# Performance work log

Measured on AMD Instinct MI355X. Metric: run time of the kernel, lower is better.

Reference implementation:

```python
import jax, jax.numpy as jnp
import numpy as np

TOKENS, HIDDEN = 2048, 1024
N_EXPERTS, INTER, TOPK = 8, 2816, 2
RENORMALIZE = True


def setup_inputs() -> dict:
    key = jax.random.key(0)
    k1, k2, k3, k4 = jax.random.split(key, 4)
    x = jax.random.normal(k1, (TOKENS, HIDDEN), dtype=jnp.float32)
    gating_output = jax.random.normal(k2, (TOKENS, N_EXPERTS), dtype=jnp.float32)
    # stacked gate_proj+up_proj per expert: [E, 2*I, H]
    w1 = jax.random.normal(k3, (N_EXPERTS, 2 * INTER, HIDDEN), dtype=jnp.float32) * 0.02
    # down_proj per expert: [E, H, I]
    w2 = jax.random.normal(k4, (N_EXPERTS, HIDDEN, INTER), dtype=jnp.float32) * 0.02
    return {"x": x, "gating_output": gating_output, "w1": w1, "w2": w2}


def _moe(x, gating_output, w1, w2):
    # fused_topk: softmax over router logits, then top-k, then renormalize
    probs = jax.nn.softmax(gating_output, axis=-1)              # [T, E]
    topk_w, topk_ids = jax.lax.top_k(probs, TOPK)                # [T, K]
    if RENORMALIZE:
        topk_w = topk_w / jnp.sum(topk_w, axis=-1, keepdims=True)
    # fused_experts: gate/up proj -> SiLU(gate)*up -> down proj, per expert
    h = jnp.einsum('th,eih->tei', x, w1)                         # [T, E, 2I]
    gate, up = h[..., :INTER], h[..., INTER:]
    act = jax.nn.silu(gate) * up                                 # [T, E, I]
    out_e = jnp.einsum('tei,ehi->teh', act, w2)                  # [T, E, H]
    # combine: gather selected experts and weight them
    sel = jnp.take_along_axis(out_e, topk_ids[:, :, None], axis=1)  # [T, K, H]
    return jnp.sum(sel * topk_w[:, :, None].astype(sel.dtype), axis=1)  # [T, H]


def reference(x, gating_output, w1, w2):
    return _moe(x, gating_output, w1, w2)
```

## Files before the change

kernel.cpp:

```cpp
#include <hip/hip_runtime.h>
#include <hip/hip_bf16.h>

#define TOKENS 2048
#define HIDDEN 1024
#define NEXP   8
#define INTER  2816
#define N1     5632
#define ROWCAP 5120
#define MT     40
#define NT1    44
#define NT2    8
#define SPLITK 2
#define CONVB  2048

typedef __attribute__((ext_vector_type(8))) short short8;
typedef __attribute__((ext_vector_type(4))) float f32x4;

typedef unsigned int __attribute__((address_space(1))) as1_uint;
typedef unsigned int __attribute__((address_space(3))) as3_uint;

__device__ __forceinline__ void gload16(const void* g, void* l) {
  __builtin_amdgcn_global_load_lds((const as1_uint*)g, (as3_uint*)l, 16, 0, 0);
}

__device__ __forceinline__ unsigned short f2bf(float f) {
  unsigned u = __float_as_uint(f);
  u += 0x7fff + ((u >> 16) & 1);
  return (unsigned short)(u >> 16);
}
__device__ __forceinline__ float bf2f(unsigned short h) {
  return __uint_as_float(((unsigned)h) << 16);
}
__device__ __forceinline__ unsigned short bfs(float x) {
  __hip_bfloat16 h = __float2bfloat16(x);
  return *reinterpret_cast<unsigned short*>(&h);
}
__device__ __forceinline__ short8 pack8(f32x4 lo, f32x4 hi) {
  short8 o;
  o[0] = (short)bfs(lo[0]); o[1] = (short)bfs(lo[1]); o[2] = (short)bfs(lo[2]); o[3] = (short)bfs(lo[3]);
  o[4] = (short)bfs(hi[0]); o[5] = (short)bfs(hi[1]); o[6] = (short)bfs(hi[2]); o[7] = (short)bfs(hi[3]);
  return o;
}

__global__ void k_routing(const float* __restrict__ gate, int* __restrict__ ctrl,
                          int* __restrict__ tkid, float* __restrict__ tkw) {
  int t = blockIdx.x * blockDim.x + threadIdx.x;
  if (t >= TOKENS) return;
  float l[8];
#pragma unroll
  for (int i = 0; i < 8; i++) l[i] = gate[t * 8 + i];
  int i0 = 0; float m0 = l[0];
#pragma unroll
  for (int i = 1; i < 8; i++) if (l[i] > m0) { m0 = l[i]; i0 = i; }
  int i1 = -1; float m1 = -3.4e38f;
#pragma unroll
  for (int i = 0; i < 8; i++) if (i != i0 && l[i] > m1) { m1 = l[i]; i1 = i; }
  float e  = __expf(m1 - m0);
  float w0 = 1.f / (1.f + e);
  float w1 = e / (1.f + e);
  tkid[2 * t] = i0; tkid[2 * t + 1] = i1;
  tkw[2 * t] = w0;  tkw[2 * t + 1] = w1;
  atomicAdd(&ctrl[i0], 1);
  atomicAdd(&ctrl[i1], 1);
}

__global__ void k_base(int* ctrl) {
  if (threadIdx.x == 0) {
    int a = 0;
    for (int e = 0; e < 8; e++) { ctrl[16 + e] = a; a += ((ctrl[e] + 127) >> 7) << 7; }
  }
}

__global__ void k_fill(int* __restrict__ ctrl, const int* __restrict__ tkid,
                       int* __restrict__ rtok, int* __restrict__ trow) {
  int t = blockIdx.x * blockDim.x + threadIdx.x;
  if (t >= TOKENS) return;
#pragma unroll
  for (int k = 0; k < 2; k++) {
    int e = tkid[2 * t + k];
    int pos = atomicAdd(&ctrl[8 + e], 1);
    int row = ctrl[16 + e] + pos;
    rtok[row] = t;
    trow[2 * t + k] = row;
  }
}

__global__ void k_prep(const float* __restrict__ x, const int* __restrict__ ctrl,
                       const int* __restrict__ rtok, unsigned short* __restrict__ Abf,
                       const float* __restrict__ w2, unsigned short* __restrict__ w2b) {
  int b = blockIdx.x;
  if (b < ROWCAP) {
    int row = b;
    int e = -1, local = 0;
    for (int i = 0; i < 8; i++) {
      int bb = ctrl[16 + i], p = ((ctrl[i] + 127) >> 7) << 7;
      if (row >= bb && row < bb + p) { e = i; local = row - bb; break; }
    }
    if (e < 0) return;
    int tid = threadIdx.x;
    unsigned short* dst = Abf + (size_t)row * HIDDEN;
    if (local < ctrl[e]) {
      int t = rtok[row];
      float4 v = ((const float4*)(x + (size_t)t * HIDDEN))[tid];
      ushort4 o; o.x = f2bf(v.x); o.y = f2bf(v.y); o.z = f2bf(v.z); o.w = f2bf(v.w);
      ((ushort4*)dst)[tid] = o;
    } else {
      ushort4 z; z.x = 0; z.y = 0; z.z = 0; z.w = 0;
      ((ushort4*)dst)[tid] = z;
    }
  } else {
    const int n8 = NEXP * HIDDEN * INTER / 8;
    int i = (b - ROWCAP) * blockDim.x + threadIdx.x;
    int stride = CONVB * blockDim.x;
    for (; i < n8; i += stride) {
      float4 a = ((const float4*)w2)[2 * i];
      float4 c = ((const float4*)w2)[2 * i + 1];
      union { ushort us[8]; uint4 v; } o;
      o.us[0] = f2bf(a.x); o.us[1] = f2bf(a.y); o.us[2] = f2bf(a.z); o.us[3] = f2bf(a.w);
      o.us[4] = f2bf(c.x); o.us[5] = f2bf(c.y); o.us[6] = f2bf(c.z); o.us[7] = f2bf(c.w);
      ((uint4*)w2b)[i] = o.v;
    }
  }
}

__device__ __forceinline__ int tile_lookup(const int* ctrl, int mt, int* ml) {
  int a0 = 0;
  for (int i = 0; i < 8; i++) {
    int pt = (ctrl[i] + 127) >> 7;
    if (mt < a0 + pt) { *ml = mt - a0; return i; }
    a0 += pt;
  }
  return -1;
}

__global__ __launch_bounds__(256, 3) void k_gemm1(const float* __restrict__ w1,
    const unsigned short* __restrict__ Abf, unsigned short* __restrict__ act,
    const int* __restrict__ ctrl) {
  union __align__(16) LdsU {
    struct { unsigned char A[16384]; unsigned char Bf[32768]; } st;
    unsigned short hb[128 * 132];
  };
  __shared__ LdsU lds;
  int bid = blockIdx.x;
  int wg = (bid & 7) * (NT1 * MT / 8) + (bid >> 3);
  int nt = wg / MT, mt = wg % MT;
  int ml; int e = tile_lookup(ctrl, mt, &ml);
  if (e < 0) return;
  int tid = threadIdx.x, lane = tid & 63, wid = tid >> 6, wr = wid >> 1, wc = wid & 1;
  int rbase = ctrl[16 + e] + ml * 128;
  const unsigned char* Ab = (const unsigned char*)(Abf + (size_t)rbase * HIDDEN);
  const unsigned char* Bw = (const unsigned char*)(w1 + (size_t)e * N1 * HIDDEN);
  int l3 = lane >> 3, l4 = lane >> 4, l15 = lane & 15;
  int swzA = ((lane & 7) ^ l3) << 4;

  unsigned aoff[4], boff[8];
#pragma unroll
  for (int i = 0; i < 4; i++) {
    int g = wid * 4 + i;
    aoff[i] = (unsigned)(g * 8 + l3) * (HIDDEN * 2) + swzA;
  }
#pragma unroll
  for (int i = 0; i < 8; i++) {
    int r = (wid * 8 + i) * 4 + l4;
    int grow = (r < 64) ? nt * 64 + r : INTER + nt * 64 + (r - 64);
    boff[i] = (unsigned)grow * (HIDDEN * 4) + ((l15 ^ (r & 15)) << 4);
  }

  f32x4 acc[4][4];
  f32x4 zero = {0.f, 0.f, 0.f, 0.f};
#pragma unroll
  for (int i = 0; i < 4; i++)
#pragma unroll
    for (int j = 0; j < 4; j++) acc[i][j] = zero;

  for (int kk = 0; kk < HIDDEN / 64; ++kk) {
#pragma unroll
    for (int i = 0; i < 4; i++)
      gload16(Ab + (size_t)aoff[i] + kk * 128, &lds.st.A[(wid * 4 + i) * 1024]);
#pragma unroll
    for (int i = 0; i < 8; i++)
      gload16(Bw + (size_t)boff[i] + kk * 256, &lds.st.Bf[(wid * 8 + i) * 1024]);
    __syncthreads();
#pragma unroll
    for (int ks = 0; ks < 2; ++ks) {
      short8 a[4], b[4];
#pragma unroll
      for (int mi = 0; mi < 4; mi++) {
        int row = wr * 64 + mi * 16 + l15;
        int koff = ks * 64 + (l4 << 4);
        a[mi] = *(const short8*)&lds.st.A[row * 128 + (koff ^ ((row & 7) << 4))];
      }
#pragma unroll
      for (int ni = 0; ni < 4; ni++) {
        int r = wc * 64 + ni * 16 + l15;
        int c = ks * 8 + l4 * 2;
        f32x4 lo = *(const f32x4*)&lds.st.Bf[r * 256 + ((c ^ (r & 15)) << 4)];
        f32x4 hi = *(const f32x4*)&lds.st.Bf[r * 256 + (((c + 1) ^ (r & 15)) << 4)];
        b[ni] = pack8(lo, hi);
      }
#pragma unroll
      for (int mi = 0; mi < 4; mi++)
#pragma unroll
        for (int ni = 0; ni < 4; ni++)
          acc[mi][ni] = __builtin_amdgcn_mfma_f32_16x16x32_bf16(a[mi], b[ni], acc[mi][ni], 0, 0, 0);
    }
    __syncthreads();
  }
#pragma unroll
  for (int mi = 0; mi < 4; mi++)
#pragma unroll
    for (int ni = 0; ni < 4; ni++)
#pragma unroll
      for (int r = 0; r < 4; r++) {
        int row = wr * 64 + mi * 16 + (l4 << 2) + r;
        int col = wc * 64 + ni * 16 + l15;
        lds.hb[row * 132 + col] = f2bf(acc[mi][ni][r]);
      }
  __syncthreads();
  {
    int r = tid >> 1, ch = (tid & 1) * 32;
    unsigned short* orow = act + (size_t)(rbase + r) * INTER + nt * 64 + ch;
    const unsigned short* hrow = &lds.hb[r * 132];
#pragma unroll
    for (int j = 0; j < 32; j += 4) {
      ushort4 o;
#pragma unroll
      for (int q = 0; q < 4; q++) {
        float g = bf2f(hrow[ch + j + q]);
        float u = bf2f(hrow[64 + ch + j + q]);
        float s = g / (1.f + __expf(-g));
        ((unsigned short*)&o)[q] = f2bf(s * u);
      }
      *(ushort4*)(orow + j) = o;
    }
  }
}

__global__ __launch_bounds__(256, 4) void k_gemm2b(const unsigned short* __restrict__ w2b,
    const unsigned short* __restrict__ act, float* __restrict__ Pb,
    const int* __restrict__ ctrl) {
  struct __align__(16) Lds2 { unsigned char A[16384]; unsigned char B[16384]; };
  __shared__ Lds2 lds;
  int bid = blockIdx.x;
  int wg = (bid & 7) * (NT2 * MT * SPLITK / 8) + (bid >> 3);
  int mt = wg % MT;
  int p = wg / MT;
  int z = p & 1, nt = p >> 1;
  int ml; int e = tile_lookup(ctrl, mt, &ml);
  if (e < 0) return;
  int tid = threadIdx.x, lane = tid & 63, wid = tid >> 6, wr = wid >> 1, wc = wid & 1;
  int rbase = ctrl[16 + e] + ml * 128;
  const int KST = (INTER / 64) / SPLITK;
  const unsigned char* Ab = (const unsigned char*)(act + (size_t)rbase * INTER) + (size_t)z * KST * 128;
  const unsigned char* Bb = (const unsigned char*)(w2b + (size_t)e * HIDDEN * INTER) + (size_t)z * KST * 128;
  int l3 = lane >> 3, l4 = lane >> 4, l15 = lane & 15;
  int swz = ((lane & 7) ^ l3) << 4;

  unsigned aoff[4], boff[4];
#pragma unroll
  for (int i = 0; i < 4; i++) {
    int g = wid * 4 + i;
    aoff[i] = (unsigned)(g * 8 + l3) * (INTER * 2) + swz;
    boff[i] = (unsigned)(nt * 128 + g * 8 + l3) * (INTER * 2) + swz;
  }

  f32x4 acc[4][4];
  f32x4 zero = {0.f, 0.f, 0.f, 0.f};
#pragma unroll
  for (int i = 0; i < 4; i++)
#pragma unroll
    for (int j = 0; j < 4; j++) acc[i][j] = zero;

  for (int kk = 0; kk < KST; ++kk) {
#pragma unroll
    for (int i = 0; i < 4; i++)
      gload16(Ab + (size_t)aoff[i] + kk * 128, &lds.A[(wid * 4 + i) * 1024]);
#pragma unroll
    for (int i = 0; i < 4; i++)
      gload16(Bb + (size_t)boff[i] + kk * 128, &lds.B[(wid * 4 + i) * 1024]);
    __syncthreads();
#pragma unroll
    for (int ks = 0; ks < 2; ++ks) {
      short8 a[4], b[4];
#pragma unroll
      for (int mi = 0; mi < 4; mi++) {
        int row = wr * 64 + mi * 16 + l15;
        int koff = ks * 64 + (l4 << 4);
        a[mi] = *(const short8*)&lds.A[row * 128 + (koff ^ ((row & 7) << 4))];
      }
#pragma unroll
      for (int ni = 0; ni < 4; ni++) {
        int row = wc * 64 + ni * 16 + l15;
        int koff = ks * 64 + (l4 << 4);
        b[ni] = *(const short8*)&lds.B[row * 128 + (koff ^ ((row & 7) << 4))];
      }
#pragma unroll
      for (int mi = 0; mi < 4; mi++)
#pragma unroll
        for (int ni = 0; ni < 4; ni++)
          acc[mi][ni] = __builtin_amdgcn_mfma_f32_16x16x32_bf16(a[mi], b[ni], acc[mi][ni], 0, 0, 0);
    }
    __syncthreads();
  }
  float* P = Pb + (size_t)z * ROWCAP * HIDDEN;
#pragma unroll
  for (int mi = 0; mi < 4; mi++)
#pragma unroll
    for (int ni = 0; ni < 4; ni++) {
      int col = nt * 128 + wc * 64 + ni * 16 + l15;
#pragma unroll
      for (int r = 0; r < 4; r++) {
        int row = rbase + wr * 64 + mi * 16 + (l4 << 2) + r;
        P[(size_t)row * HIDDEN + col] = acc[mi][ni][r];
      }
    }
}

__global__ void k_finish(const float* __restrict__ Pb,
                         const int* __restrict__ trow, const float* __restrict__ tkw,
                         float* __restrict__ out) {
  int t = blockIdx.x, c = threadIdx.x;
  const float* P0 = Pb;
  const float* P1 = Pb + (size_t)ROWCAP * HIDDEN;
  int r0 = trow[2 * t], r1 = trow[2 * t + 1];
  float w0 = tkw[2 * t], w1 = tkw[2 * t + 1];
  float4 a0 = ((const float4*)(P0 + (size_t)r0 * HIDDEN))[c];
  float4 b0 = ((const float4*)(P1 + (size_t)r0 * HIDDEN))[c];
  float4 a1 = ((const float4*)(P0 + (size_t)r1 * HIDDEN))[c];
  float4 b1 = ((const float4*)(P1 + (size_t)r1 * HIDDEN))[c];
  float4 o;
  o.x = w0 * (a0.x + b0.x) + w1 * (a1.x + b1.x);
  o.y = w0 * (a0.y + b0.y) + w1 * (a1.y + b1.y);
  o.z = w0 * (a0.z + b0.z) + w1 * (a1.z + b1.z);
  o.w = w0 * (a0.w + b0.w) + w1 * (a1.w + b1.w);
  ((float4*)(out + (size_t)t * HIDDEN))[c] = o;
}

extern "C" void kernel_launch(void* const* d_in, const int* in_sizes, int n_in,
                              void* d_out, int out_size, void* d_ws, size_t ws_size,
                              hipStream_t stream) {
  const float* x      = (const float*)d_in[0];
  const float* gating = (const float*)d_in[1];
  const float* w1     = (const float*)d_in[2];
  const float* w2     = (const float*)d_in[3];
  float* out = (float*)d_out;
  char* ws = (char*)d_ws;

  int*   ctrl = (int*)ws;
  int*   tkid = (int*)(ws + 4096);
  float* tkw  = (float*)(ws + 24576);
  int*   rtok = (int*)(ws + 45056);
  int*   trow = (int*)(ws + 73728);
  size_t off_Abf = 131072;
  size_t off_act = off_Abf + (size_t)ROWCAP * HIDDEN * 2;
  size_t off_w2b = off_act + (size_t)ROWCAP * INTER * 2;
  size_t off_P   = off_w2b + (size_t)NEXP * HIDDEN * INTER * 2;
  unsigned short* Abf  = (unsigned short*)(ws + off_Abf);
  unsigned short* actb = (unsigned short*)(ws + off_act);
  unsigned short* w2b  = (unsigned short*)(ws + off_w2b);
  float* Pb = (float*)(ws + off_P);

  hipMemsetAsync(ws, 0, 1024, stream);

  k_routing<<<TOKENS / 256, 256, 0, stream>>>(gating, ctrl, tkid, tkw);
  k_base<<<1, 64, 0, stream>>>(ctrl);
  k_fill<<<TOKENS / 256, 256, 0, stream>>>(ctrl, tkid, rtok, trow);
  k_prep<<<ROWCAP + CONVB, 256, 0, stream>>>(x, ctrl, rtok, Abf, w2, w2b);
  k_gemm1<<<NT1 * MT, 256, 0, stream>>>(w1, Abf, actb, ctrl);
  k_gemm2b<<<NT2 * MT * SPLITK, 256, 0, stream>>>(w2b, actb, Pb, ctrl);
  k_finish<<<TOKENS, 256, 0, stream>>>(Pb, trow, tkw, out);
}
```

Baseline: 246.4 us.

## Increase down-proj split-K to four and fold expert base computation inline

Doubles the split-K factor of the second expert GEMM to create more workgroups, and raises its occupancy hint. The finish kernel now sums an arbitrary number of partial buffers. The separate k_base launch is removed; expert row bases are recomputed from counts inside the consumer kernels. The trade is more fp32 partial-sum traffic and workspace in exchange for parallelism and one less launch.

```diff
diff --git a/kernel.cpp b/kernel.cpp
--- a/kernel.cpp
+++ b/kernel.cpp
@@ -10,7 +10,7 @@
 #define MT     40
 #define NT1    44
 #define NT2    8
-#define SPLITK 2
+#define SPLITK 4
 #define CONVB  2048
 
 typedef __attribute__((ext_vector_type(8))) short short8;
@@ -64,11 +64,10 @@
   atomicAdd(&ctrl[i1], 1);
 }
 
-__global__ void k_base(int* ctrl) {
-  if (threadIdx.x == 0) {
-    int a = 0;
-    for (int e = 0; e < 8; e++) { ctrl[16 + e] = a; a += ((ctrl[e] + 127) >> 7) << 7; }
-  }
+__device__ __forceinline__ int base_of(const int* __restrict__ cnt, int e) {
+  int a = 0;
+  for (int i = 0; i < e; i++) a += ((cnt[i] + 127) >> 7) << 7;
+  return a;
 }
 
 __global__ void k_fill(int* __restrict__ ctrl, const int* __restrict__ tkid,
@@ -79,7 +78,7 @@
   for (int k = 0; k < 2; k++) {
     int e = tkid[2 * t + k];
     int pos = atomicAdd(&ctrl[8 + e], 1);
-    int row = ctrl[16 + e] + pos;
+    int row = base_of(ctrl, e) + pos;
     rtok[row] = t;
     trow[2 * t + k] = row;
   }
@@ -91,10 +90,11 @@
   int b = blockIdx.x;
   if (b < ROWCAP) {
     int row = b;
-    int e = -1, local = 0;
+    int e = -1, local = 0, b0 = 0;
     for (int i = 0; i < 8; i++) {
-      int bb = ctrl[16 + i], p = ((ctrl[i] + 127) >> 7) << 7;
-      if (row >= bb && row < bb + p) { e = i; local = row - bb; break; }
+      int p = ((ctrl[i] + 127) >> 7) << 7;
+      if (row >= b0 && row < b0 + p) { e = i; local = row - b0; break; }
+      b0 += p;
     }
     if (e < 0) return;
     int tid = threadIdx.x;
@@ -123,12 +123,12 @@
   }
 }
 
-__device__ __forceinline__ int tile_lookup(const int* ctrl, int mt, int* ml) {
-  int a0 = 0;
+__device__ __forceinline__ int tile_lookup2(const int* ctrl, int mt, int* ml, int* rb) {
+  int a0 = 0, b0 = 0;
   for (int i = 0; i < 8; i++) {
     int pt = (ctrl[i] + 127) >> 7;
-    if (mt < a0 + pt) { *ml = mt - a0; return i; }
-    a0 += pt;
+    if (mt < a0 + pt) { *ml = mt - a0; *rb = b0; return i; }
+    a0 += pt; b0 += pt << 7;
   }
   return -1;
 }
@@ -144,10 +144,10 @@
   int bid = blockIdx.x;
   int wg = (bid & 7) * (NT1 * MT / 8) + (bid >> 3);
   int nt = wg / MT, mt = wg % MT;
-  int ml; int e = tile_lookup(ctrl, mt, &ml);
+  int ml, rb; int e = tile_lookup2(ctrl, mt, &ml, &rb);
   if (e < 0) return;
   int tid = threadIdx.x, lane = tid & 63, wid = tid >> 6, wr = wid >> 1, wc = wid & 1;
-  int rbase = ctrl[16 + e] + ml * 128;
+  int rbase = rb + ml * 128;
   const unsigned char* Ab = (const unsigned char*)(Abf + (size_t)rbase * HIDDEN);
   const unsigned char* Bw = (const unsigned char*)(w1 + (size_t)e * N1 * HIDDEN);
   int l3 = lane >> 3, l4 = lane >> 4, l15 = lane & 15;
@@ -236,7 +236,7 @@
   }
 }
 
-__global__ __launch_bounds__(256, 4) void k_gemm2b(const unsigned short* __restrict__ w2b,
+__global__ __launch_bounds__(256, 5) void k_gemm2b(const unsigned short* __restrict__ w2b,
     const unsigned short* __restrict__ act, float* __restrict__ Pb,
     const int* __restrict__ ctrl) {
   struct __align__(16) Lds2 { unsigned char A[16384]; unsigned char B[16384]; };
@@ -245,11 +245,11 @@
   int wg = (bid & 7) * (NT2 * MT * SPLITK / 8) + (bid >> 3);
   int mt = wg % MT;
   int p = wg / MT;
-  int z = p & 1, nt = p >> 1;
-  int ml; int e = tile_lookup(ctrl, mt, &ml);
+  int z = p & 3, nt = p >> 2;
+  int ml, rb; int e = tile_lookup2(ctrl, mt, &ml, &rb);
   if (e < 0) return;
   int tid = threadIdx.x, lane = tid & 63, wid = tid >> 6, wr = wid >> 1, wc = wid & 1;
-  int rbase = ctrl[16 + e] + ml * 128;
+  int rbase = rb + ml * 128;
   const int KST = (INTER / 64) / SPLITK;
   const unsigned char* Ab = (const unsigned char*)(act + (size_t)rbase * INTER) + (size_t)z * KST * 128;
   const unsigned char* Bb = (const unsigned char*)(w2b + (size_t)e * HIDDEN * INTER) + (size_t)z * KST * 128;
@@ -320,19 +320,22 @@
                          const int* __restrict__ trow, const float* __restrict__ tkw,
                          float* __restrict__ out) {
   int t = blockIdx.x, c = threadIdx.x;
-  const float* P0 = Pb;
-  const float* P1 = Pb + (size_t)ROWCAP * HIDDEN;
   int r0 = trow[2 * t], r1 = trow[2 * t + 1];
   float w0 = tkw[2 * t], w1 = tkw[2 * t + 1];
-  float4 a0 = ((const float4*)(P0 + (size_t)r0 * HIDDEN))[c];
-  float4 b0 = ((const float4*)(P1 + (size_t)r0 * HIDDEN))[c];
-  float4 a1 = ((const float4*)(P0 + (size_t)r1 * HIDDEN))[c];
-  float4 b1 = ((const float4*)(P1 + (size_t)r1 * HIDDEN))[c];
+  float4 s0 = {0.f, 0.f, 0.f, 0.f}, s1 = {0.f, 0.f, 0.f, 0.f};
+#pragma unroll
+  for (int z = 0; z < SPLITK; z++) {
+    const float* P = Pb + (size_t)z * ROWCAP * HIDDEN;
+    float4 a = ((const float4*)(P + (size_t)r0 * HIDDEN))[c];
+    float4 b = ((const float4*)(P + (size_t)r1 * HIDDEN))[c];
+    s0.x += a.x; s0.y += a.y; s0.z += a.z; s0.w += a.w;
+    s1.x += b.x; s1.y += b.y; s1.z += b.z; s1.w += b.w;
+  }
   float4 o;
-  o.x = w0 * (a0.x + b0.x) + w1 * (a1.x + b1.x);
-  o.y = w0 * (a0.y + b0.y) + w1 * (a1.y + b1.y);
-  o.z = w0 * (a0.z + b0.z) + w1 * (a1.z + b1.z);
-  o.w = w0 * (a0.w + b0.w) + w1 * (a1.w + b1.w);
+  o.x = w0 * s0.x + w1 * s1.x;
+  o.y = w0 * s0.y + w1 * s1.y;
+  o.z = w0 * s0.z + w1 * s1.z;
+  o.w = w0 * s0.w + w1 * s1.w;
   ((float4*)(out + (size_t)t * HIDDEN))[c] = o;
 }
 
@@ -363,7 +366,6 @@
   hipMemsetAsync(ws, 0, 1024, stream);
 
   k_routing<<<TOKENS / 256, 256, 0, stream>>>(gating, ctrl, tkid, tkw);
-  k_base<<<1, 64, 0, stream>>>(ctrl);
   k_fill<<<TOKENS / 256, 256, 0, stream>>>(ctrl, tkid, rtok, trow);
   k_prep<<<ROWCAP + CONVB, 256, 0, stream>>>(x, ctrl, rtok, Abf, w2, w2b);
   k_gemm1<<<NT1 * MT, 256, 0, stream>>>(w1, Abf, actb, ctrl);
```

Result: slower. 361.5 us (+46.7%).
